# Kernel optimization log

Hardware: AMD Instinct MI355X
Metric: run time of the kernel (lower is better)

The kernel has to match this reference:

```python
import jax, jax.numpy as jnp
import numpy as np

N, D, E, H = 1024, 256, 16, 8
HD = D // H
F = 4 * D  # GatedMLP intermediate
SCALE = 1.0 / np.sqrt(HD)
EPS = 1e-6


def rmsnorm(x, w):
    rms = jnp.sqrt(jnp.mean(x * x, axis=-1, keepdims=True) + EPS)
    return x / rms * w


def mha(x, wq, wk, wv, wo, mask=None, edge_bias=None):
    # x: [N, D]; weights stored (in, out) so y = x @ W
    q = (x @ wq).reshape(N, H, HD).transpose(1, 0, 2)  # [H, N, HD]
    k = (x @ wk).reshape(N, H, HD).transpose(1, 0, 2)
    v = (x @ wv).reshape(N, H, HD).transpose(1, 0, 2)
    scores = jnp.einsum('hnd,hmd->hnm', q, k) * SCALE  # [H, N, N]
    if edge_bias is not None:
        scores = scores + edge_bias.transpose(2, 0, 1)
    if mask is not None:
        scores = jnp.where(mask[None, :, :], scores, -jnp.inf)
    attn = jax.nn.softmax(scores, axis=-1)
    attn = jnp.nan_to_num(attn, nan=0.0)
    out = jnp.einsum('hnm,hmd->hnd', attn, v)  # [H, N, HD]
    out = out.transpose(1, 0, 2).reshape(N, D)
    return out @ wo


def setup_inputs() -> dict:
    key = jax.random.key(0)
    ks = jax.random.split(key, 40)
    i = iter(range(40))

    def g(shape, s=0.02):
        return (jax.random.normal(ks[next(i)], shape) * s).astype(jnp.float32)

    inp = {
        'features': jax.random.normal(ks[next(i)], (N, D), dtype=jnp.float32),
        'adjacency': jax.random.randint(ks[next(i)], (N, N), 0, 2, dtype=jnp.int32),
        'edge_features': jax.random.normal(ks[next(i)], (N, N, E), dtype=jnp.float32),
        'role_indices': jax.random.randint(ks[next(i)], (N,), 0, 16, dtype=jnp.int64),
        'role_norm_w': jnp.ones((D,), jnp.float32),
        'role_q_w': g((D, D)), 'role_k_w': g((D, D)), 'role_v_w': g((D, D)), 'role_o_w': g((D, D)),
        'nb_norm_w': jnp.ones((D,), jnp.float32),
        'nb_q_w': g((D, D)), 'nb_k_w': g((D, D)), 'nb_v_w': g((D, D)), 'nb_o_w': g((D, D)),
        'edge_w1': g((E, D)), 'edge_b1': jnp.zeros((D,), jnp.float32),
        'edge_w2': g((D, H)), 'edge_b2': jnp.zeros((H,), jnp.float32),
        'full_norm_w': jnp.ones((D,), jnp.float32),
        'full_q_w': g((D, D)), 'full_k_w': g((D, D)), 'full_v_w': g((D, D)), 'full_o_w': g((D, D)),
        'feat_norm_w': jnp.ones((D,), jnp.float32),
        'feat_t_w': g((D, D)), 'feat_t_b': jnp.zeros((D,), jnp.float32),
        'feat_g_w': g((2 * D, D)), 'feat_g_b': jnp.zeros((D,), jnp.float32),
        'ffn_norm_w': jnp.ones((D,), jnp.float32),
        'ffn_gate_w': g((D, F)), 'ffn_up_w': g((D, F)), 'ffn_down_w': g((F, D)),
    }
    return inp


def reference(features, adjacency, edge_features, role_indices,
              role_norm_w, role_q_w, role_k_w, role_v_w, role_o_w,
              nb_norm_w, nb_q_w, nb_k_w, nb_v_w, nb_o_w,
              edge_w1, edge_b1, edge_w2, edge_b2,
              full_norm_w, full_q_w, full_k_w, full_v_w, full_o_w,
              feat_norm_w, feat_t_w, feat_t_b, feat_g_w, feat_g_b,
              ffn_norm_w, ffn_gate_w, ffn_up_w, ffn_down_w):
    # masks (dropout is identity in eval mode)
    role_mask = role_indices[:, None] == role_indices[None, :]          # [N, N]
    neighbor_mask = (adjacency > 0) | jnp.eye(N, dtype=bool)            # [N, N]

    x = features
    # 1. role attention
    x = x + mha(rmsnorm(x, role_norm_w), role_q_w, role_k_w, role_v_w, role_o_w, mask=role_mask)
    # 2. neighbor attention with per-head edge bias from MLP over edge features
    hdn = jax.nn.silu(edge_features @ edge_w1 + edge_b1)                # [N, N, D]
    edge_bias = hdn @ edge_w2 + edge_b2                                 # [N, N, H]
    x = x + mha(rmsnorm(x, nb_norm_w), nb_q_w, nb_k_w, nb_v_w, nb_o_w, mask=neighbor_mask, edge_bias=edge_bias)
    # 3. full attention
    x = x + mha(rmsnorm(x, full_norm_w), full_q_w, full_k_w, full_v_w, full_o_w)
    # 4. feature mixing (gated residual)
    xn = rmsnorm(x, feat_norm_w)
    t = jax.nn.silu(xn @ feat_t_w + feat_t_b)
    gate = jax.nn.sigmoid(jnp.concatenate([xn, t], axis=-1) @ feat_g_w + feat_g_b)
    x = x + gate * t
    # 5. gated FFN
    xn = rmsnorm(x, ffn_norm_w)
    x = x + (jax.nn.silu(xn @ ffn_gate_w) * (xn @ ffn_up_w)) @ ffn_down_w
    return x
```

## Files before the change

kernel.cpp:

```cpp
#include <hip/hip_runtime.h>
#include <math.h>

#define N 1024
#define D 256
#define E 16
#define H 8
#define HD 32
#define F 1024
#define NN (1024 * 1024)
#define SCALE 0.17677669529663687f
#define EPS 1e-6f

typedef unsigned short u16;
typedef __attribute__((ext_vector_type(8))) short bfrag8;
typedef __attribute__((ext_vector_type(4))) float accf4;

__device__ __forceinline__ float block_sum(float v) {
    #pragma unroll
    for (int off = 32; off > 0; off >>= 1) v += __shfl_xor(v, off);
    __shared__ float ws[4];
    if ((threadIdx.x & 63) == 0) ws[threadIdx.x >> 6] = v;
    __syncthreads();
    v = ws[0] + ws[1] + ws[2] + ws[3];
    __syncthreads();
    return v;
}

__device__ __forceinline__ float silu_f(float x) { return x / (1.f + __expf(-x)); }
__device__ __forceinline__ float sigmoid_f(float x) { return 1.f / (1.f + __expf(-x)); }

__device__ __forceinline__ u16 f2bf(float x) {
    union { float f; unsigned int u; } c;
    c.f = x;
    unsigned int r = c.u + 0x7fffu + ((c.u >> 16) & 1u);
    return (u16)(r >> 16);
}

__device__ __forceinline__ float bf2f(u16 v) {
    union { unsigned int u; float f; } c;
    c.u = ((unsigned int)v) << 16;
    return c.f;
}

__device__ __forceinline__ unsigned int cvt_pk_bf16(float a, float b) {
    unsigned int r;
    asm("v_cvt_pk_bf16_f32 %0, %1, %2" : "=v"(r) : "v"(a), "v"(b));
    return r;
}

__global__ void copy4_kernel(const float4* __restrict__ a, float4* __restrict__ b, int n4) {
    int i = blockIdx.x * 256 + threadIdx.x;
    if (i < n4) b[i] = a[i];
}

__global__ void gate_combine_kernel(const float* __restrict__ g, const u16* __restrict__ t,
                                    float* __restrict__ x, int n) {
    int i = blockIdx.x * 256 + threadIdx.x;
    if (i < n) x[i] += sigmoid_f(g[i]) * bf2f(t[i]);
}

__global__ void ffn_mulcvt_kernel(const u16* __restrict__ guv, u16* __restrict__ hb) {
    int i = blockIdx.x * 256 + threadIdx.x;
    int j = i >> 10, f = i & 1023;
    float g = bf2f(guv[(long)j * 2048 + f]);
    float u = bf2f(guv[(long)j * 2048 + 1024 + f]);
    hb[i] = f2bf(silu_f(g) * u);
}

__global__ void rmsnorm_bf16_kernel(const float* __restrict__ x, const float* __restrict__ w,
                                    u16* __restrict__ out) {
    int row = blockIdx.x;
    int t = threadIdx.x;
    float v = x[(long)row * D + t];
    float s = block_sum(v * v);
    float rms = sqrtf(s * (1.f / D) + EPS);
    out[(long)row * D + t] = f2bf(v / rms * w[t]);
}

__global__ void transpose_bf16_kernel(const float* __restrict__ in, long ldin,
                                      u16* __restrict__ out, int K, int Nc) {
    __shared__ float tile[32][33];
    int k0 = blockIdx.y * 32, n0 = blockIdx.x * 32;
    int c = threadIdx.x & 31, r8 = threadIdx.x >> 5;
    #pragma unroll
    for (int i = 0; i < 4; i++) {
        int r = r8 + i * 8;
        tile[r][c] = in[(long)(k0 + r) * ldin + n0 + c];
    }
    __syncthreads();
    #pragma unroll
    for (int i = 0; i < 4; i++) {
        int r = r8 + i * 8;
        out[(long)(n0 + r) * K + k0 + c] = f2bf(tile[c][r]);
    }
}

struct Src15 { const float* p[15]; };
__global__ void transpose15_kernel(Src15 srcs, u16* __restrict__ wall) {
    __shared__ float tile[32][33];
    const float* in = srcs.p[blockIdx.z];
    u16* out = wall + (size_t)blockIdx.z * 65536;
    int k0 = blockIdx.y * 32, n0 = blockIdx.x * 32;
    int c = threadIdx.x & 31, r8 = threadIdx.x >> 5;
    #pragma unroll
    for (int i = 0; i < 4; i++) {
        int r = r8 + i * 8;
        tile[r][c] = in[(long)(k0 + r) * 256 + n0 + c];
    }
    __syncthreads();
    #pragma unroll
    for (int i = 0; i < 4; i++) {
        int r = r8 + i * 8;
        out[(long)(n0 + r) * 256 + k0 + c] = f2bf(tile[c][r]);
    }
}

struct Src2 { const float* p[2]; };
__global__ void transpose_gu_kernel(Src2 srcs, u16* __restrict__ wgut) {
    __shared__ float tile[32][33];
    const float* in = srcs.p[blockIdx.z];
    u16* out = wgut + (size_t)blockIdx.z * (size_t)F * 256;
    int k0 = blockIdx.y * 32, n0 = blockIdx.x * 32;
    int c = threadIdx.x & 31, r8 = threadIdx.x >> 5;
    #pragma unroll
    for (int i = 0; i < 4; i++) {
        int r = r8 + i * 8;
        tile[r][c] = in[(long)(k0 + r) * F + n0 + c];
    }
    __syncthreads();
    #pragma unroll
    for (int i = 0; i < 4; i++) {
        int r = r8 + i * 8;
        out[(long)(n0 + r) * 256 + k0 + c] = f2bf(tile[c][r]);
    }
}

__global__ void transpose_u16_kernel(const u16* __restrict__ in, long ldin,
                                     u16* __restrict__ out, int K, int Nc) {
    __shared__ u16 tile[32][34];
    int k0 = blockIdx.y * 32, n0 = blockIdx.x * 32;
    int c = threadIdx.x & 31, r8 = threadIdx.x >> 5;
    #pragma unroll
    for (int i = 0; i < 4; i++) {
        int r = r8 + i * 8;
        tile[r][c] = in[(long)(k0 + r) * ldin + n0 + c];
    }
    __syncthreads();
    #pragma unroll
    for (int i = 0; i < 4; i++) {
        int r = r8 + i * 8;
        out[(long)(n0 + r) * K + k0 + c] = tile[c][r];
    }
}

template <int NTW, int ACT, bool ACCUM, bool BIAS, bool BF16O>
__global__ __launch_bounds__(256) void bgemm_kernel(
    const u16* __restrict__ A, const u16* __restrict__ B, const float* __restrict__ bias,
    void* __restrict__ C, int M, int K, int Nc, int ldc, long sA, long sB, long sC) {
    constexpr int NTILE = NTW * 16;
    __shared__ __align__(16) u16 Asm[64 * 72];
    __shared__ __align__(16) u16 Bsm[NTILE * 72];
    A += (long)blockIdx.z * sA;
    B += (long)blockIdx.z * sB;
    long cbase = (long)blockIdx.z * sC;
    int m0 = blockIdx.y * 64, n0 = blockIdx.x * NTILE;
    int t = threadIdx.x;
    int wave = t >> 6, lane = t & 63, lg = lane >> 4, lr = lane & 15;
    accf4 acc[NTW] = {};
    for (int k0 = 0; k0 < K; k0 += 64) {
        #pragma unroll
        for (int c = 0; c < 2; c++) {
            int flat = c * 4096 + t * 16;
            int row = flat >> 7, col = (flat & 127) >> 1;
            *(int4*)&Asm[row * 72 + col] = *(const int4*)&A[(long)(m0 + row) * K + k0 + col];
        }
        #pragma unroll
        for (int c = 0; c < NTW / 2; c++) {
            int flat = c * 4096 + t * 16;
            int row = flat >> 7, col = (flat & 127) >> 1;
            *(int4*)&Bsm[row * 72 + col] = *(const int4*)&B[(long)(n0 + row) * K + k0 + col];
        }
        __syncthreads();
        #pragma unroll
        for (int ks = 0; ks < 2; ks++) {
            bfrag8 af = *(const bfrag8*)&Asm[(wave * 16 + lr) * 72 + ks * 32 + lg * 8];
            #pragma unroll
            for (int nt = 0; nt < NTW; nt++) {
                bfrag8 bf = *(const bfrag8*)&Bsm[(nt * 16 + lr) * 72 + ks * 32 + lg * 8];
                acc[nt] = __builtin_amdgcn_mfma_f32_16x16x32_bf16(af, bf, acc[nt], 0, 0, 0);
            }
        }
        __syncthreads();
    }
    float* Cf = (float*)C;
    u16* Cb = (u16*)C;
    #pragma unroll
    for (int nt = 0; nt < NTW; nt++) {
        int gn = n0 + nt * 16 + lr;
        #pragma unroll
        for (int r = 0; r < 4; r++) {
            int gm = m0 + wave * 16 + lg * 4 + r;
            float v = acc[nt][r];
            if (BIAS) v += bias[gn];
            if (ACT == 1) v = silu_f(v);
            long idx = cbase + (long)gm * ldc + gn;
            if (BF16O) Cb[idx] = f2bf(v);
            else if (ACCUM) Cf[idx] += v;
            else Cf[idx] = v;
        }
    }
}

template <int MASK>
__global__ __launch_bounds__(256) void flash_attn_kernel(
    const u16* __restrict__ qkvbf, const u16* __restrict__ vbt,
    const float* __restrict__ ebT, const int* __restrict__ roles,
    const int* __restrict__ adj, u16* __restrict__ aob) {
    __shared__ int roles_s[N];
    __shared__ __align__(16) u16 P_lds[4][16][72];
    __shared__ float mrg_m[4][16], mrg_l[4][16];
    __shared__ __align__(16) float mrg_O[2][32][16];

    int h = blockIdx.y;
    int t = threadIdx.x, wave = t >> 6, lane = t & 63;
    int lg = lane >> 4, lr = lane & 15;
    int iw = wave >> 1, jh = wave & 1;
    int i = blockIdx.x * 32 + iw * 16 + lr;

    if (MASK == 1) {
        #pragma unroll
        for (int c = 0; c < 4; c++) roles_s[t + c * 256] = roles[t + c * 256];
    }
    __syncthreads();

    bfrag8 qf = *(const bfrag8*)&qkvbf[(long)i * 768 + h * HD + lg * 8];
    int role_i = (MASK == 1) ? roles_s[i] : 0;

    accf4 o0 = {0.f, 0.f, 0.f, 0.f}, o1 = {0.f, 0.f, 0.f, 0.f};
    float m_run = -1e30f, l_run = 0.f;

    for (int jt = 0; jt < 8; jt++) {
        int j0 = jh * 512 + jt * 64;
        float p[16];
        float tmax = -1e30f;
        #pragma unroll
        for (int js = 0; js < 4; js++) {
            bfrag8 kf = *(const bfrag8*)&qkvbf[(long)(j0 + js * 16 + lr) * 768 + 256 + h * HD + lg * 8];
            accf4 z = {0.f, 0.f, 0.f, 0.f};
            accf4 s = __builtin_amdgcn_mfma_f32_16x16x32_bf16(kf, qf, z, 0, 0, 0);
            float4 eb4;
            int4 ad4;
            if (MASK == 2) {
                eb4 = *(const float4*)&ebT[(long)h * NN + (long)i * N + j0 + js * 16 + lg * 4];
                ad4 = *(const int4*)&adj[(long)i * N + j0 + js * 16 + lg * 4];
            }
            #pragma unroll
            for (int r = 0; r < 4; r++) {
                int j = j0 + js * 16 + lg * 4 + r;
                float val = s[r] * SCALE;
                bool keep = true;
                if (MASK == 2) {
                    val += (r == 0) ? eb4.x : (r == 1) ? eb4.y : (r == 2) ? eb4.z : eb4.w;
                    int av = (r == 0) ? ad4.x : (r == 1) ? ad4.y : (r == 2) ? ad4.z : ad4.w;
                    keep = (av > 0) || (i == j);
                }
                if (MASK == 1) keep = (roles_s[j] == role_i);
                val = keep ? val : -1e30f;
                p[js * 4 + r] = val;
                tmax = fmaxf(tmax, val);
            }
        }
        tmax = fmaxf(tmax, __shfl_xor(tmax, 16));
        tmax = fmaxf(tmax, __shfl_xor(tmax, 32));
        float m_new = fmaxf(m_run, tmax);
        float alpha = __expf(m_run - m_new);
        float lsum = 0.f;
        #pragma unroll
        for (int v = 0; v < 16; v++) {
            float pe = __expf(p[v] - m_new);
            p[v] = pe;
            lsum += pe;
        }
        lsum += __shfl_xor(lsum, 16);
        lsum += __shfl_xor(lsum, 32);
        l_run = l_run * alpha + lsum;
        m_run = m_new;
        #pragma unroll
        for (int r = 0; r < 4; r++) { o0[r] *= alpha; o1[r] *= alpha; }
        #pragma unroll
        for (int js = 0; js < 4; js++) {
            uint2 pk;
            pk.x = cvt_pk_bf16(p[js * 4 + 0], p[js * 4 + 1]);
            pk.y = cvt_pk_bf16(p[js * 4 + 2], p[js * 4 + 3]);
            *(uint2*)&P_lds[wave][lr][js * 16 + lg * 4] = pk;
        }
        #pragma unroll
        for (int ks = 0; ks < 2; ks++) {
            bfrag8 pb = *(const bfrag8*)&P_lds[wave][lr][ks * 32 + lg * 8];
            bfrag8 v0 = *(const bfrag8*)&vbt[(long)(h * HD + lr) * N + j0 + ks * 32 + lg * 8];
            bfrag8 v1 = *(const bfrag8*)&vbt[(long)(h * HD + 16 + lr) * N + j0 + ks * 32 + lg * 8];
            o0 = __builtin_amdgcn_mfma_f32_16x16x32_bf16(v0, pb, o0, 0, 0, 0);
            o1 = __builtin_amdgcn_mfma_f32_16x16x32_bf16(v1, pb, o1, 0, 0, 0);
        }
    }

    if (lg == 0) { mrg_m[wave][lr] = m_run; mrg_l[wave][lr] = l_run; }
    __syncthreads();
    int other = wave ^ 1;
    float m_o = mrg_m[other][lr], l_o = mrg_l[other][lr];
    float m_tot = fmaxf(m_run, m_o);
    float a_s = __expf(m_run - m_tot);
    float a_o = __expf(m_o - m_tot);
    float inv = 1.f / (a_s * l_run + a_o * l_o);
    if (jh == 0) {
        #pragma unroll
        for (int r = 0; r < 4; r++) {
            mrg_O[iw][lg * 4 + r][lr] = a_s * o0[r];
            mrg_O[iw][16 + lg * 4 + r][lr] = a_s * o1[r];
        }
    }
    __syncthreads();
    if (jh == 1) {
        #pragma unroll
        for (int r = 0; r < 4; r++) {
            float f0 = (mrg_O[iw][lg * 4 + r][lr] + a_s * o0[r]) * inv;
            float f1 = (mrg_O[iw][16 + lg * 4 + r][lr] + a_s * o1[r]) * inv;
            aob[(long)i * D + h * HD + lg * 4 + r] = f2bf(f0);
            aob[(long)i * D + h * HD + 16 + lg * 4 + r] = f2bf(f1);
        }
    }
}

__global__ __launch_bounds__(256) void edge_mlp_mfma_kernel(
    const float* __restrict__ ef, const float* __restrict__ w1, const float* __restrict__ b1,
    const float* __restrict__ w2, const float* __restrict__ b2, float* __restrict__ ebT) {
    __shared__ __align__(16) u16 smem[4][16 * 264];
    u16* w1t = &smem[0][0];
    u16* w2t = w1t + 4096;
    int t = threadIdx.x;
    int i = blockIdx.x;

    {
        int d = t;
        #pragma unroll
        for (int e = 0; e < 16; e++) w1t[d * 16 + e] = f2bf(w1[e * 256 + d]);
        float4 wa = *(const float4*)&w2[d * 8];
        float4 wb = *(const float4*)&w2[d * 8 + 4];
        w2t[0 * 256 + d] = f2bf(wa.x);
        w2t[1 * 256 + d] = f2bf(wa.y);
        w2t[2 * 256 + d] = f2bf(wa.z);
        w2t[3 * 256 + d] = f2bf(wa.w);
        w2t[4 * 256 + d] = f2bf(wb.x);
        w2t[5 * 256 + d] = f2bf(wb.y);
        w2t[6 * 256 + d] = f2bf(wb.z);
        w2t[7 * 256 + d] = f2bf(wb.w);
        #pragma unroll
        for (int h = 8; h < 16; h++) w2t[h * 256 + d] = 0;
    }
    __syncthreads();

    int wave = t >> 6, lane = t & 63;
    int lg = lane >> 4, lr = lane & 15;

    bfrag8 a1[16];
    #pragma unroll
    for (int dt = 0; dt < 16; dt++) {
        int d = dt * 16 + lr;
        if (lg < 2) {
            a1[dt] = *(const bfrag8*)&w1t[d * 16 + lg * 8];
        } else if (lg == 2) {
            union { unsigned int u[4]; bfrag8 s; } z = {{0u, 0u, 0u, 0u}};
            z.u[0] = (unsigned int)f2bf(b1[d]);
            a1[dt] = z.s;
        } else {
            union { unsigned int u[4]; bfrag8 s; } z = {{0u, 0u, 0u, 0u}};
            a1[dt] = z.s;
        }
    }
    bfrag8 a2[8];
    #pragma unroll
    for (int ks = 0; ks < 8; ks++)
        a2[ks] = *(const bfrag8*)&w2t[lr * 256 + ks * 32 + lg * 8];

    float b2v[4];
    #pragma unroll
    for (int r = 0; r < 4; r++) b2v[r] = (lg < 2) ? b2[lg * 4 + r] : 0.f;

    __syncthreads();
    u16* hw = smem[wave];

    float4 f0, f1;
    if (lg < 2) {
        const float* p = &ef[((long)i * N + wave * 16 + lr) * E + lg * 8];
        f0 = *(const float4*)p;
        f1 = *(const float4*)(p + 4);
    }

    for (int it = 0; it < 16; it++) {
        long rowbase = (long)i * N + (it * 4 + wave) * 16;
        bfrag8 bfrag;
        if (lg < 2) {
            union { unsigned int u[4]; bfrag8 s; } uu;
            uu.u[0] = cvt_pk_bf16(f0.x, f0.y);
            uu.u[1] = cvt_pk_bf16(f0.z, f0.w);
            uu.u[2] = cvt_pk_bf16(f1.x, f1.y);
            uu.u[3] = cvt_pk_bf16(f1.z, f1.w);
            bfrag = uu.s;
        } else {
            union { unsigned int u[4]; bfrag8 s; } uu = {{(lg == 2) ? 0x3f80u : 0u, 0u, 0u, 0u}};
            bfrag = uu.s;
        }
        if (it < 15 && lg < 2) {
            const float* p = &ef[((long)i * N + ((it + 1) * 4 + wave) * 16 + lr) * E + lg * 8];
            f0 = *(const float4*)p;
            f1 = *(const float4*)(p + 4);
        }
        #pragma unroll
        for (int dt = 0; dt < 16; dt++) {
            accf4 acc = {0.f, 0.f, 0.f, 0.f};
            acc = __builtin_amdgcn_mfma_f32_16x16x32_bf16(a1[dt], bfrag, acc, 0, 0, 0);
            float s0 = silu_f(acc[0]);
            float s1 = silu_f(acc[1]);
            float s2 = silu_f(acc[2]);
            float s3 = silu_f(acc[3]);
            uint2 pk;
            pk.x = cvt_pk_bf16(s0, s1);
            pk.y = cvt_pk_bf16(s2, s3);
            *(uint2*)&hw[lr * 264 + dt * 16 + lg * 4] = pk;
        }
        bfrag8 hbv[8];
        #pragma unroll
        for (int ks = 0; ks < 8; ks++)
            hbv[ks] = *(const bfrag8*)&hw[lr * 264 + ks * 32 + lg * 8];
        accf4 acc2 = {0.f, 0.f, 0.f, 0.f};
        #pragma unroll
        for (int ks = 0; ks < 8; ks++)
            acc2 = __builtin_amdgcn_mfma_f32_16x16x32_bf16(a2[ks], hbv[ks], acc2, 0, 0, 0);
        if (lg < 2) {
            #pragma unroll
            for (int r = 0; r < 4; r++)
                ebT[(long)(lg * 4 + r) * NN + rowbase + lr] = acc2[r] + b2v[r];
        }
    }
}

extern "C" void kernel_launch(void* const* d_in, const int* in_sizes, int n_in,
                              void* d_out, int out_size, void* d_ws, size_t ws_size,
                              hipStream_t stream) {
    const float* features   = (const float*)d_in[0];
    const int*   adjacency  = (const int*)d_in[1];
    const float* edge_feats = (const float*)d_in[2];
    const int*   role_idx   = (const int*)d_in[3];
    const float* role_norm_w = (const float*)d_in[4];
    const float* role_q_w = (const float*)d_in[5];
    const float* role_k_w = (const float*)d_in[6];
    const float* role_v_w = (const float*)d_in[7];
    const float* role_o_w = (const float*)d_in[8];
    const float* nb_norm_w = (const float*)d_in[9];
    const float* nb_q_w = (const float*)d_in[10];
    const float* nb_k_w = (const float*)d_in[11];
    const float* nb_v_w = (const float*)d_in[12];
    const float* nb_o_w = (const float*)d_in[13];
    const float* edge_w1 = (const float*)d_in[14];
    const float* edge_b1 = (const float*)d_in[15];
    const float* edge_w2 = (const float*)d_in[16];
    const float* edge_b2 = (const float*)d_in[17];
    const float* full_norm_w = (const float*)d_in[18];
    const float* full_q_w = (const float*)d_in[19];
    const float* full_k_w = (const float*)d_in[20];
    const float* full_v_w = (const float*)d_in[21];
    const float* full_o_w = (const float*)d_in[22];
    const float* feat_norm_w = (const float*)d_in[23];
    const float* feat_t_w = (const float*)d_in[24];
    const float* feat_t_b = (const float*)d_in[25];
    const float* feat_g_w = (const float*)d_in[26];
    const float* feat_g_b = (const float*)d_in[27];
    const float* ffn_norm_w = (const float*)d_in[28];
    const float* ffn_gate_w = (const float*)d_in[29];
    const float* ffn_up_w = (const float*)d_in[30];
    const float* ffn_down_w = (const float*)d_in[31];

    char* wsp = (char*)d_ws;
    size_t off = 0;
    auto alloc = [&](size_t bytes) -> void* {
        void* p = wsp + off;
        off += (bytes + 255) & ~(size_t)255;
        return p;
    };
    float* x    = (float*)alloc((size_t)N * D * 4);
    float* tmp  = (float*)alloc((size_t)N * D * 4);
    float* eb   = (float*)alloc((size_t)H * NN * 4);
    u16* qkvbf = (u16*)alloc((size_t)N * 768 * 2);
    u16* guvb = (u16*)alloc((size_t)N * 2048 * 2);
    u16* aob  = (u16*)alloc((size_t)N * D * 2);
    u16* xnb  = (u16*)alloc((size_t)N * D * 2);
    u16* tb   = (u16*)alloc((size_t)N * D * 2);
    u16* hb   = (u16*)alloc((size_t)N * F * 2);
    u16* vbt  = (u16*)alloc((size_t)D * N * 2);
    u16* wall = (u16*)alloc((size_t)15 * 65536 * 2);
    u16* wgut = (u16*)alloc((size_t)2048 * 256 * 2);
    u16* wdt  = (u16*)alloc((size_t)256 * 1024 * 2);

    u16* wqkvt[3], *wot[3];
    for (int a = 0; a < 3; a++) {
        wqkvt[a] = wall + (size_t)(a * 4) * 65536;
        wot[a]   = wall + (size_t)(a * 4 + 3) * 65536;
    }
    u16* wtt  = wall + (size_t)12 * 65536;
    u16* wg1t = wall + (size_t)13 * 65536;
    u16* wg2t = wall + (size_t)14 * 65536;

    Src15 s15;
    s15.p[0] = role_q_w;  s15.p[1] = role_k_w;  s15.p[2] = role_v_w;  s15.p[3] = role_o_w;
    s15.p[4] = nb_q_w;    s15.p[5] = nb_k_w;    s15.p[6] = nb_v_w;    s15.p[7] = nb_o_w;
    s15.p[8] = full_q_w;  s15.p[9] = full_k_w;  s15.p[10] = full_v_w; s15.p[11] = full_o_w;
    s15.p[12] = feat_t_w; s15.p[13] = feat_g_w; s15.p[14] = feat_g_w + (size_t)D * D;
    transpose15_kernel<<<dim3(8, 8, 15), 256, 0, stream>>>(s15, wall);
    Src2 s2;
    s2.p[0] = ffn_gate_w; s2.p[1] = ffn_up_w;
    transpose_gu_kernel<<<dim3(32, 8, 2), 256, 0, stream>>>(s2, wgut);
    transpose_bf16_kernel<<<dim3(8, 32), 256, 0, stream>>>(ffn_down_w, D, wdt, F, D);

    copy4_kernel<<<(N * D / 4) / 256, 256, 0, stream>>>((const float4*)features, (float4*)x, N * D / 4);
    edge_mlp_mfma_kernel<<<N, 256, 0, stream>>>(edge_feats, edge_w1, edge_b1, edge_w2, edge_b2, eb);

    const float* nw[3] = {role_norm_w, nb_norm_w, full_norm_w};
    dim3 fgrid(N / 32, H);

    for (int a = 0; a < 3; a++) {
        rmsnorm_bf16_kernel<<<N, 256, 0, stream>>>(x, nw[a], xnb);
        bgemm_kernel<4, 0, false, false, true><<<dim3(768 / 64, N / 64, 1), 256, 0, stream>>>(
            xnb, wqkvt[a], nullptr, qkvbf, N, 256, 768, 768, 0, 0, 0);
        transpose_u16_kernel<<<dim3(8, 32), 256, 0, stream>>>(qkvbf + 512, 768, vbt, N, D);
        if (a == 0)
            flash_attn_kernel<1><<<fgrid, 256, 0, stream>>>(qkvbf, vbt, nullptr, role_idx, nullptr, aob);
        else if (a == 1)
            flash_attn_kernel<2><<<fgrid, 256, 0, stream>>>(qkvbf, vbt, eb, nullptr, adjacency, aob);
        else
            flash_attn_kernel<0><<<fgrid, 256, 0, stream>>>(qkvbf, vbt, nullptr, nullptr, nullptr, aob);
        bgemm_kernel<4, 0, true, false, false><<<dim3(D / 64, N / 64, 1), 256, 0, stream>>>(
            aob, wot[a], nullptr, x, N, 256, D, D, 0, 0, 0);
    }

    rmsnorm_bf16_kernel<<<N, 256, 0, stream>>>(x, feat_norm_w, xnb);
    bgemm_kernel<4, 1, false, true, true><<<dim3(D / 64, N / 64, 1), 256, 0, stream>>>(
        xnb, wtt, feat_t_b, tb, N, 256, D, D, 0, 0, 0);
    bgemm_kernel<4, 0, false, true, false><<<dim3(D / 64, N / 64, 1), 256, 0, stream>>>(
        xnb, wg1t, feat_g_b, tmp, N, 256, D, D, 0, 0, 0);
    bgemm_kernel<4, 0, true, false, false><<<dim3(D / 64, N / 64, 1), 256, 0, stream>>>(
        tb, wg2t, nullptr, tmp, N, 256, D, D, 0, 0, 0);
    gate_combine_kernel<<<(N * D) / 256, 256, 0, stream>>>(tmp, tb, x, N * D);

    rmsnorm_bf16_kernel<<<N, 256, 0, stream>>>(x, ffn_norm_w, xnb);
    bgemm_kernel<4, 0, false, false, true><<<dim3(2048 / 64, N / 64, 1), 256, 0, stream>>>(
        xnb, wgut, nullptr, guvb, N, 256, 2048, 2048, 0, 0, 0);
    ffn_mulcvt_kernel<<<(N * F) / 256, 256, 0, stream>>>(guvb, hb);
    bgemm_kernel<4, 0, true, false, false><<<dim3(D / 64, N / 64, 1), 256, 0, stream>>>(
        hb, wdt, nullptr, x, N, 1024, D, D, 0, 0, 0);
    copy4_kernel<<<(N * D / 4) / 256, 256, 0, stream>>>((const float4*)x, (float4*)d_out, N * D / 4);
}
```

Before: 491.4 us.

## Fuse elementwise epilogues into GEMMs and store edge bias in bf16

Removes the copy, gate-combine and FFN mul/convert kernels by folding them into GEMM epilogues. The gate GEMM now runs over the concatenated [xn, t] buffer with a single K=512 pass, and the gate/up weights are interleaved so one tile holds both halves for the silu*up step. The residual source is read directly, so the initial and final copies go away, and the edge-bias tensor is stored in bf16 to halve its traffic in the neighbor attention. This trades some precision in the edge bias for fewer launches and less memory traffic.

```diff
diff --git a/kernel.cpp b/kernel.cpp
--- a/kernel.cpp
+++ b/kernel.cpp
@@ -48,33 +48,14 @@
     return r;
 }
 
-__global__ void copy4_kernel(const float4* __restrict__ a, float4* __restrict__ b, int n4) {
-    int i = blockIdx.x * 256 + threadIdx.x;
-    if (i < n4) b[i] = a[i];
-}
-
-__global__ void gate_combine_kernel(const float* __restrict__ g, const u16* __restrict__ t,
-                                    float* __restrict__ x, int n) {
-    int i = blockIdx.x * 256 + threadIdx.x;
-    if (i < n) x[i] += sigmoid_f(g[i]) * bf2f(t[i]);
-}
-
-__global__ void ffn_mulcvt_kernel(const u16* __restrict__ guv, u16* __restrict__ hb) {
-    int i = blockIdx.x * 256 + threadIdx.x;
-    int j = i >> 10, f = i & 1023;
-    float g = bf2f(guv[(long)j * 2048 + f]);
-    float u = bf2f(guv[(long)j * 2048 + 1024 + f]);
-    hb[i] = f2bf(silu_f(g) * u);
-}
-
 __global__ void rmsnorm_bf16_kernel(const float* __restrict__ x, const float* __restrict__ w,
-                                    u16* __restrict__ out) {
+                                    u16* __restrict__ out, int ldo) {
     int row = blockIdx.x;
     int t = threadIdx.x;
     float v = x[(long)row * D + t];
     float s = block_sum(v * v);
     float rms = sqrtf(s * (1.f / D) + EPS);
-    out[(long)row * D + t] = f2bf(v / rms * w[t]);
+    out[(long)row * ldo + t] = f2bf(v / rms * w[t]);
 }
 
 __global__ void transpose_bf16_kernel(const float* __restrict__ in, long ldin,
@@ -119,19 +100,20 @@
 __global__ void transpose_gu_kernel(Src2 srcs, u16* __restrict__ wgut) {
     __shared__ float tile[32][33];
     const float* in = srcs.p[blockIdx.z];
-    u16* out = wgut + (size_t)blockIdx.z * (size_t)F * 256;
-    int k0 = blockIdx.y * 32, n0 = blockIdx.x * 32;
+    int zoff = blockIdx.z * 32;
+    int k0 = blockIdx.y * 32, f0 = blockIdx.x * 32;
     int c = threadIdx.x & 31, r8 = threadIdx.x >> 5;
     #pragma unroll
     for (int i = 0; i < 4; i++) {
         int r = r8 + i * 8;
-        tile[r][c] = in[(long)(k0 + r) * F + n0 + c];
-    }
-    __syncthreads();
-    #pragma unroll
-    for (int i = 0; i < 4; i++) {
-        int r = r8 + i * 8;
-        out[(long)(n0 + r) * 256 + k0 + c] = f2bf(tile[c][r]);
+        tile[r][c] = in[(long)(k0 + r) * F + f0 + c];
+    }
+    __syncthreads();
+    #pragma unroll
+    for (int i = 0; i < 4; i++) {
+        int r = r8 + i * 8;
+        int rnew = (f0 >> 5) * 64 + zoff + r;
+        wgut[(long)rnew * 256 + k0 + c] = f2bf(tile[c][r]);
     }
 }
 
@@ -153,10 +135,11 @@
     }
 }
 
-template <int NTW, int ACT, bool ACCUM, bool BIAS, bool BF16O>
+template <int NTW, int ACT, bool ACCUM, bool BIAS, bool BF16O, bool SRC>
 __global__ __launch_bounds__(256) void bgemm_kernel(
     const u16* __restrict__ A, const u16* __restrict__ B, const float* __restrict__ bias,
-    void* __restrict__ C, int M, int K, int Nc, int ldc, long sA, long sB, long sC) {
+    void* __restrict__ C, const float* __restrict__ csrc, const u16* __restrict__ gt, int ldg,
+    int M, int K, int lda, int Nc, int ldc, long sA, long sB, long sC) {
     constexpr int NTILE = NTW * 16;
     __shared__ __align__(16) u16 Asm[64 * 72];
     __shared__ __align__(16) u16 Bsm[NTILE * 72];
@@ -172,7 +155,7 @@
         for (int c = 0; c < 2; c++) {
             int flat = c * 4096 + t * 16;
             int row = flat >> 7, col = (flat & 127) >> 1;
-            *(int4*)&Asm[row * 72 + col] = *(const int4*)&A[(long)(m0 + row) * K + k0 + col];
+            *(int4*)&Asm[row * 72 + col] = *(const int4*)&A[(long)(m0 + row) * lda + k0 + col];
         }
         #pragma unroll
         for (int c = 0; c < NTW / 2; c++) {
@@ -194,19 +177,35 @@
     }
     float* Cf = (float*)C;
     u16* Cb = (u16*)C;
-    #pragma unroll
-    for (int nt = 0; nt < NTW; nt++) {
-        int gn = n0 + nt * 16 + lr;
-        #pragma unroll
-        for (int r = 0; r < 4; r++) {
-            int gm = m0 + wave * 16 + lg * 4 + r;
-            float v = acc[nt][r];
-            if (BIAS) v += bias[gn];
-            if (ACT == 1) v = silu_f(v);
-            long idx = cbase + (long)gm * ldc + gn;
-            if (BF16O) Cb[idx] = f2bf(v);
-            else if (ACCUM) Cf[idx] += v;
-            else Cf[idx] = v;
+    if (ACT == 3) {
+        #pragma unroll
+        for (int nt = 0; nt < 2; nt++) {
+            int fcol = (n0 >> 1) + nt * 16 + lr;
+            #pragma unroll
+            for (int r = 0; r < 4; r++) {
+                int gm = m0 + wave * 16 + lg * 4 + r;
+                float g = acc[nt][r];
+                float u = acc[nt + 2][r];
+                Cb[(long)gm * ldc + fcol] = f2bf(silu_f(g) * u);
+            }
+        }
+    } else {
+        #pragma unroll
+        for (int nt = 0; nt < NTW; nt++) {
+            int gn = n0 + nt * 16 + lr;
+            #pragma unroll
+            for (int r = 0; r < 4; r++) {
+                int gm = m0 + wave * 16 + lg * 4 + r;
+                float v = acc[nt][r];
+                if (BIAS) v += bias[gn];
+                if (ACT == 1) v = silu_f(v);
+                if (ACT == 2) v = sigmoid_f(v) * bf2f(gt[(long)gm * ldg + gn]);
+                long idx = cbase + (long)gm * ldc + gn;
+                if (BF16O) Cb[idx] = f2bf(v);
+                else if (SRC) Cf[idx] = csrc[idx] + v;
+                else if (ACCUM) Cf[idx] += v;
+                else Cf[idx] = v;
+            }
         }
     }
 }
@@ -214,7 +213,7 @@
 template <int MASK>
 __global__ __launch_bounds__(256) void flash_attn_kernel(
     const u16* __restrict__ qkvbf, const u16* __restrict__ vbt,
-    const float* __restrict__ ebT, const int* __restrict__ roles,
+    const u16* __restrict__ ebTb, const int* __restrict__ roles,
     const int* __restrict__ adj, u16* __restrict__ aob) {
     __shared__ int roles_s[N];
     __shared__ __align__(16) u16 P_lds[4][16][72];
@@ -248,10 +247,10 @@
             bfrag8 kf = *(const bfrag8*)&qkvbf[(long)(j0 + js * 16 + lr) * 768 + 256 + h * HD + lg * 8];
             accf4 z = {0.f, 0.f, 0.f, 0.f};
             accf4 s = __builtin_amdgcn_mfma_f32_16x16x32_bf16(kf, qf, z, 0, 0, 0);
-            float4 eb4;
+            uint2 e2;
             int4 ad4;
             if (MASK == 2) {
-                eb4 = *(const float4*)&ebT[(long)h * NN + (long)i * N + j0 + js * 16 + lg * 4];
+                e2 = *(const uint2*)&ebTb[(long)h * NN + (long)i * N + j0 + js * 16 + lg * 4];
                 ad4 = *(const int4*)&adj[(long)i * N + j0 + js * 16 + lg * 4];
             }
             #pragma unroll
@@ -260,7 +259,8 @@
                 float val = s[r] * SCALE;
                 bool keep = true;
                 if (MASK == 2) {
-                    val += (r == 0) ? eb4.x : (r == 1) ? eb4.y : (r == 2) ? eb4.z : eb4.w;
+                    unsigned int w = (r < 2) ? e2.x : e2.y;
+                    val += bf2f((u16)(w >> ((r & 1) * 16)));
                     int av = (r == 0) ? ad4.x : (r == 1) ? ad4.y : (r == 2) ? ad4.z : ad4.w;
                     keep = (av > 0) || (i == j);
                 }
@@ -333,7 +333,7 @@
 
 __global__ __launch_bounds__(256) void edge_mlp_mfma_kernel(
     const float* __restrict__ ef, const float* __restrict__ w1, const float* __restrict__ b1,
-    const float* __restrict__ w2, const float* __restrict__ b2, float* __restrict__ ebT) {
+    const float* __restrict__ w2, const float* __restrict__ b2, u16* __restrict__ ebTb) {
     __shared__ __align__(16) u16 smem[4][16 * 264];
     u16* w1t = &smem[0][0];
     u16* w2t = w1t + 4096;
@@ -439,7 +439,7 @@
         if (lg < 2) {
             #pragma unroll
             for (int r = 0; r < 4; r++)
-                ebT[(long)(lg * 4 + r) * NN + rowbase + lr] = acc2[r] + b2v[r];
+                ebTb[(long)(lg * 4 + r) * NN + rowbase + lr] = f2bf(acc2[r] + b2v[r]);
         }
     }
 }
@@ -488,16 +488,15 @@
         return p;
     };
     float* x    = (float*)alloc((size_t)N * D * 4);
-    float* tmp  = (float*)alloc((size_t)N * D * 4);
-    float* eb   = (float*)alloc((size_t)H * NN * 4);
+    u16* ebb  = (u16*)alloc((size_t)H * NN * 2);
     u16* qkvbf = (u16*)alloc((size_t)N * 768 * 2);
-    u16* guvb = (u16*)alloc((size_t)N * 2048 * 2);
     u16* aob  = (u16*)alloc((size_t)N * D * 2);
     u16* xnb  = (u16*)alloc((size_t)N * D * 2);
-    u16* tb   = (u16*)alloc((size_t)N * D * 2);
+    u16* xnt  = (u16*)alloc((size_t)N * 512 * 2);
     u16* hb   = (u16*)alloc((size_t)N * F * 2);
     u16* vbt  = (u16*)alloc((size_t)D * N * 2);
     u16* wall = (u16*)alloc((size_t)15 * 65536 * 2);
+    u16* wgt  = (u16*)alloc((size_t)256 * 512 * 2);
     u16* wgut = (u16*)alloc((size_t)2048 * 256 * 2);
     u16* wdt  = (u16*)alloc((size_t)256 * 1024 * 2);
 
@@ -506,56 +505,54 @@
         wqkvt[a] = wall + (size_t)(a * 4) * 65536;
         wot[a]   = wall + (size_t)(a * 4 + 3) * 65536;
     }
-    u16* wtt  = wall + (size_t)12 * 65536;
-    u16* wg1t = wall + (size_t)13 * 65536;
-    u16* wg2t = wall + (size_t)14 * 65536;
+    u16* wtt = wall + (size_t)12 * 65536;
 
     Src15 s15;
     s15.p[0] = role_q_w;  s15.p[1] = role_k_w;  s15.p[2] = role_v_w;  s15.p[3] = role_o_w;
     s15.p[4] = nb_q_w;    s15.p[5] = nb_k_w;    s15.p[6] = nb_v_w;    s15.p[7] = nb_o_w;
     s15.p[8] = full_q_w;  s15.p[9] = full_k_w;  s15.p[10] = full_v_w; s15.p[11] = full_o_w;
-    s15.p[12] = feat_t_w; s15.p[13] = feat_g_w; s15.p[14] = feat_g_w + (size_t)D * D;
-    transpose15_kernel<<<dim3(8, 8, 15), 256, 0, stream>>>(s15, wall);
+    s15.p[12] = feat_t_w; s15.p[13] = feat_t_w; s15.p[14] = feat_t_w;
+    transpose15_kernel<<<dim3(8, 8, 13), 256, 0, stream>>>(s15, wall);
+    transpose_bf16_kernel<<<dim3(8, 16), 256, 0, stream>>>(feat_g_w, D, wgt, 512, D);
     Src2 s2;
     s2.p[0] = ffn_gate_w; s2.p[1] = ffn_up_w;
     transpose_gu_kernel<<<dim3(32, 8, 2), 256, 0, stream>>>(s2, wgut);
     transpose_bf16_kernel<<<dim3(8, 32), 256, 0, stream>>>(ffn_down_w, D, wdt, F, D);
 
-    copy4_kernel<<<(N * D / 4) / 256, 256, 0, stream>>>((const float4*)features, (float4*)x, N * D / 4);
-    edge_mlp_mfma_kernel<<<N, 256, 0, stream>>>(edge_feats, edge_w1, edge_b1, edge_w2, edge_b2, eb);
+    edge_mlp_mfma_kernel<<<N, 256, 0, stream>>>(edge_feats, edge_w1, edge_b1, edge_w2, edge_b2, ebb);
 
     const float* nw[3] = {role_norm_w, nb_norm_w, full_norm_w};
+    const float* xsrc0 = features;
     dim3 fgrid(N / 32, H);
 
     for (int a = 0; a < 3; a++) {
-        rmsnorm_bf16_kernel<<<N, 256, 0, stream>>>(x, nw[a], xnb);
-        bgemm_kernel<4, 0, false, false, true><<<dim3(768 / 64, N / 64, 1), 256, 0, stream>>>(
-            xnb, wqkvt[a], nullptr, qkvbf, N, 256, 768, 768, 0, 0, 0);
+        rmsnorm_bf16_kernel<<<N, 256, 0, stream>>>(a == 0 ? features : x, nw[a], xnb, 256);
+        bgemm_kernel<4, 0, false, false, true, false><<<dim3(768 / 64, N / 64, 1), 256, 0, stream>>>(
+            xnb, wqkvt[a], nullptr, qkvbf, nullptr, nullptr, 0, N, 256, 256, 768, 768, 0, 0, 0);
         transpose_u16_kernel<<<dim3(8, 32), 256, 0, stream>>>(qkvbf + 512, 768, vbt, N, D);
         if (a == 0)
             flash_attn_kernel<1><<<fgrid, 256, 0, stream>>>(qkvbf, vbt, nullptr, role_idx, nullptr, aob);
         else if (a == 1)
-            flash_attn_kernel<2><<<fgrid, 256, 0, stream>>>(qkvbf, vbt, eb, nullptr, adjacency, aob);
+            flash_attn_kernel<2><<<fgrid, 256, 0, stream>>>(qkvbf, vbt, ebb, nullptr, adjacency, aob);
         else
             flash_attn_kernel<0><<<fgrid, 256, 0, stream>>>(qkvbf, vbt, nullptr, nullptr, nullptr, aob);
-        bgemm_kernel<4, 0, true, false, false><<<dim3(D / 64, N / 64, 1), 256, 0, stream>>>(
-            aob, wot[a], nullptr, x, N, 256, D, D, 0, 0, 0);
-    }
-
-    rmsnorm_bf16_kernel<<<N, 256, 0, stream>>>(x, feat_norm_w, xnb);
-    bgemm_kernel<4, 1, false, true, true><<<dim3(D / 64, N / 64, 1), 256, 0, stream>>>(
-        xnb, wtt, feat_t_b, tb, N, 256, D, D, 0, 0, 0);
-    bgemm_kernel<4, 0, false, true, false><<<dim3(D / 64, N / 64, 1), 256, 0, stream>>>(
-        xnb, wg1t, feat_g_b, tmp, N, 256, D, D, 0, 0, 0);
-    bgemm_kernel<4, 0, true, false, false><<<dim3(D / 64, N / 64, 1), 256, 0, stream>>>(
-        tb, wg2t, nullptr, tmp, N, 256, D, D, 0, 0, 0);
-    gate_combine_kernel<<<(N * D) / 256, 256, 0, stream>>>(tmp, tb, x, N * D);
-
-    rmsnorm_bf16_kernel<<<N, 256, 0, stream>>>(x, ffn_norm_w, xnb);
-    bgemm_kernel<4, 0, false, false, true><<<dim3(2048 / 64, N / 64, 1), 256, 0, stream>>>(
-        xnb, wgut, nullptr, guvb, N, 256, 2048, 2048, 0, 0, 0);
-    ffn_mulcvt_kernel<<<(N * F) / 256, 256, 0, stream>>>(guvb, hb);
-    bgemm_kernel<4, 0, true, false, false><<<dim3(D / 64, N / 64, 1), 256, 0, stream>>>(
-        hb, wdt, nullptr, x, N, 1024, D, D, 0, 0, 0);
-    copy4_kernel<<<(N * D / 4) / 256, 256, 0, stream>>>((const float4*)x, (float4*)d_out, N * D / 4);
-}
+        if (a == 0)
+            bgemm_kernel<4, 0, false, false, false, true><<<dim3(D / 64, N / 64, 1), 256, 0, stream>>>(
+                aob, wot[a], nullptr, x, xsrc0, nullptr, 0, N, 256, 256, D, D, 0, 0, 0);
+        else
+            bgemm_kernel<4, 0, true, false, false, false><<<dim3(D / 64, N / 64, 1), 256, 0, stream>>>(
+                aob, wot[a], nullptr, x, nullptr, nullptr, 0, N, 256, 256, D, D, 0, 0, 0);
+    }
+
+    rmsnorm_bf16_kernel<<<N, 256, 0, stream>>>(x, feat_norm_w, xnt, 512);
+    bgemm_kernel<4, 1, false, true, true, false><<<dim3(D / 64, N / 64, 1), 256, 0, stream>>>(
+        xnt, wtt, feat_t_b, xnt + 256, nullptr, nullptr, 0, N, 256, 512, D, 512, 0, 0, 0);
+    bgemm_kernel<4, 2, true, true, false, false><<<dim3(D / 64, N / 64, 1), 256, 0, stream>>>(
+        xnt, wgt, feat_g_b, x, nullptr, xnt + 256, 512, N, 512, 512, D, D, 0, 0, 0);
+
+    rmsnorm_bf16_kernel<<<N, 256, 0, stream>>>(x, ffn_norm_w, xnb, 256);
+    bgemm_kernel<4, 3, false, false, true, false><<<dim3(2048 / 64, N / 64, 1), 256, 0, stream>>>(
+        xnb, wgut, nullptr, hb, nullptr, nullptr, 0, N, 256, 256, 2048, F, 0, 0, 0);
+    bgemm_kernel<4, 0, false, false, false, true><<<dim3(D / 64, N / 64, 1), 256, 0, stream>>>(
+        hb, wdt, nullptr, d_out, x, nullptr, 0, N, 1024, 1024, D, D, 0, 0, 0);
+}
```

Result: faster. 481.3 us (-2.1%).
